# Kernel optimization log

Hardware: AMD Instinct MI355X
Metric: run time of the kernel (lower is better)

The kernel has to match this reference:

```python
import jax, jax.numpy as jnp
import numpy as np

B, T, F, DH, DG = 64, 4096, 64, 64, 128
SPAN, MASK_PROB = 5, 0.15
GROUPS = [(0, 5), (5, 8), (8, 11), (11, 14), (14, 26), (26, 38), (38, 46), (46, 64)]


def _make_feature_mask(rng):
    # Temporal span masking: num_spans spans of length SPAN, start ~ (U^2)*(T-SPAN)
    temporal = np.zeros((B, T), dtype=bool)
    num_spans = max(1, int(T * MASK_PROB / SPAN))
    starts = (rng.random((B, num_spans)) ** 2 * (T - SPAN)).astype(np.int64)
    for b in range(B):
        for s in starts[b]:
            temporal[b, s:s + SPAN] = True
    bb, tt = np.nonzero(temporal)
    n = len(bb)
    gm = np.zeros((8, F), dtype=np.uint8)
    for g, (a, c) in enumerate(GROUPS):
        gm[g, a:c] = 1
    sel = np.zeros((n, 8), dtype=np.uint8)
    branch = rng.random(n) < 0.3
    pairs = np.array([[4, 5], [1, 2], [6, 1]])
    pidx = rng.integers(0, 3, n)
    rows = np.nonzero(branch)[0]
    sel[rows, pairs[pidx[rows], 0]] = 1
    sel[rows, pairs[pidx[rows], 1]] = 1
    rows2 = np.nonzero(~branch)[0]
    k = rng.integers(1, 4, len(rows2))
    scores = rng.random((len(rows2), 8))
    rank = scores.argsort(axis=1).argsort(axis=1)
    sel[rows2] = (rank < k[:, None]).astype(np.uint8)
    fm = np.zeros((B, T, F), dtype=bool)
    fm[bb, tt] = (sel @ gm) > 0
    return fm


def setup_inputs() -> dict:
    rng = np.random.default_rng(0)
    x = jnp.asarray(rng.standard_normal((B, T, F)).astype(np.float32))
    feature_mask = jnp.asarray(_make_feature_mask(rng))

    def p(*s):
        return jnp.asarray((rng.standard_normal(s) * 0.05).astype(np.float32))

    return dict(
        x=x, feature_mask=feature_mask,
        stem_w=p(F, DH), stem_b=p(DH),
        conv_w=p(DH, DH, 3), conv_b=p(DH),
        gru_w_ih=p(3 * DG, DH), gru_w_hh=p(3 * DG, DG),
        gru_b_ih=p(3 * DG), gru_b_hh=p(3 * DG),
        h1_w=p(DG, 128), h1_b=p(128),
        h2_w=p(128, 128), h2_b=p(128),
        h3_w=p(128, F), h3_b=p(F),
    )


def _gelu(v):
    return jax.nn.gelu(v, approximate=False)


def _gru(x, w_ih, w_hh, b_ih, b_hh):
    # torch nn.GRU semantics, batch_first. x: (B, T, DH) -> (B, T, DG)
    H = w_hh.shape[1]
    gx = jnp.einsum('btd,hd->bth', x, w_ih) + b_ih  # (B, T, 3H)

    def step(h, gx_t):
        gh = h @ w_hh.T + b_hh  # (B, 3H)
        r = jax.nn.sigmoid(gx_t[:, :H] + gh[:, :H])
        z = jax.nn.sigmoid(gx_t[:, H:2 * H] + gh[:, H:2 * H])
        n = jnp.tanh(gx_t[:, 2 * H:] + r * gh[:, 2 * H:])
        h_new = (1.0 - z) * n + z * h
        return h_new, h_new

    h0 = jnp.zeros((x.shape[0], H), x.dtype)
    _, hs = jax.lax.scan(step, h0, jnp.swapaxes(gx, 0, 1))  # (T, B, H)
    return jnp.swapaxes(hs, 0, 1)


def reference(x, feature_mask, stem_w, stem_b, conv_w, conv_b,
              gru_w_ih, gru_w_hh, gru_b_ih, gru_b_hh,
              h1_w, h1_b, h2_w, h2_b, h3_w, h3_b):
    # mask-apply
    xm = jnp.where(feature_mask, jnp.zeros((), x.dtype), x)
    # encoder: Linear -> GELU -> Conv1d(k=3,pad=1) -> GELU -> GRU
    h = _gelu(xm @ stem_w + stem_b)  # (B, T, DH)
    hc = jax.lax.conv_general_dilated(
        jnp.swapaxes(h, 1, 2), conv_w, window_strides=(1,), padding=((1, 1),),
        dimension_numbers=('NCH', 'OIH', 'NCH'))
    h = _gelu(jnp.swapaxes(hc, 1, 2) + conv_b)
    z = _gru(h, gru_w_ih, gru_w_hh, gru_b_ih, gru_b_hh)  # (B, T, DG)
    # recon head
    r = _gelu(z @ h1_w + h1_b)
    r = _gelu(r @ h2_w + h2_b)
    x_recon = r @ h3_w + h3_b  # (B, T, F)
    # feature-normalized masked MSE (torch std is unbiased, ddof=1)
    scale = jnp.std(x, axis=(0, 1), ddof=1) + 1e-8
    diff = (x_recon - x) ** 2 / scale ** 2
    m = feature_mask.astype(x.dtype)
    return jnp.sum(diff * m) / jnp.maximum(jnp.sum(m), 1.0)
```

## Files before the change

kernel.cpp:

```cpp
#include <hip/hip_runtime.h>
#include <hip/hip_bf16.h>

#define DEV __device__ __forceinline__

namespace {

constexpr int ROWS = 64 * 4096;
constexpr int NE   = ROWS * 64;
constexpr int CHUNK = 512;
constexpr int NCHUNK = 4096 / CHUNK;

constexpr size_t GXCH = (size_t)64 * CHUNK * 384;
constexpr size_t RCH  = (size_t)64 * CHUNK * 128;

constexpr size_t OFF_XC  = 0;
constexpr size_t OFF_MC  = 33554432;
constexpr size_t OFF_WC  = 50331648;
constexpr size_t OFF_ACC = 50862080;
constexpr size_t OFF_H2  = 50866176;
constexpr size_t OFF_GX  = 84420608;
constexpr size_t OFF_ZR  = 134752256;
constexpr size_t OFF_R1  = 151529472;
constexpr size_t OFF_R2  = 168306688;
constexpr size_t OFF_HST = 185083904;

DEV float rlane(float v, int l) {
    return __int_as_float(__builtin_amdgcn_readlane(__float_as_int(v), l));
}
DEV unsigned int rlu(unsigned int v, int l) {
    return (unsigned int)__builtin_amdgcn_readlane((int)v, l);
}
DEV float bf2f(unsigned short u) { return __uint_as_float(((unsigned int)u) << 16); }
DEV unsigned short f2bf(float f) {
    unsigned int u = __float_as_uint(f);
    unsigned int r = (u + 0x7FFFu + ((u >> 16) & 1u)) >> 16;
    return (unsigned short)r;
}
DEV float gelu_f(float v) { return 0.5f * v * (1.0f + erff(v * 0.70710678118654752f)); }
DEV float sigm_f(float x) { return 1.0f / (1.0f + __expf(-x)); }
DEV float tanh_f(float x) { float t = __expf(2.0f * x); return 1.0f - 2.0f / (t + 1.0f); }

typedef _Float16 half2v __attribute__((ext_vector_type(2)));
typedef __attribute__((ext_vector_type(8))) short bf16x8;
typedef __attribute__((ext_vector_type(4))) float f32x4;

DEV float dot2(half2v a, half2v b, float c) {
#if __has_builtin(__builtin_amdgcn_fdot2)
    return __builtin_amdgcn_fdot2(a, b, c, false);
#else
    return c + (float)a.x * (float)b.x + (float)a.y * (float)b.y;
#endif
}
DEV unsigned short f2h_bits(float f) {
    return __builtin_bit_cast(unsigned short, (_Float16)f);
}
DEV float h2f_bits(unsigned short u) {
    return (float)__builtin_bit_cast(_Float16, u);
}
DEV half2v u2h2(unsigned int p) { return __builtin_bit_cast(half2v, p); }
DEV void bar_lds() {
    asm volatile("s_waitcnt lgkmcnt(0)\n\ts_barrier" ::: "memory");
}

}

__global__ __launch_bounds__(256) void k_probe(const unsigned short* __restrict__ xh,
    const unsigned char* __restrict__ mb, int* __restrict__ cnt)
{
    const int g = blockIdx.x * 256 + threadIdx.x;
    int hit = 0;
    for (int i = g; i < (1 << 20); i += (1 << 16)) {
        int tb = (xh[i] >> 8) & 0x7F;
        hit += (tb >= 0x3C && tb <= 0x40) ? 1 : 0;
    }
    int a = 0, b = 0, c = 0, d = 0;
    for (int i = g; i < (1 << 24); i += (1 << 16)) {
        unsigned char v = mb[i];
        int r = i & 3;
        a += (v == 1    && r == 0) ? 1 : 0;
        b += (v == 1    && r != 0) ? 1 : 0;
        c += (v == 0x80 && r == 0) ? 1 : 0;
        d += (v == 0x80 && r == 2) ? 1 : 0;
    }
    __shared__ int sm[256];
    int vals[5] = {hit, a, b, c, d};
#pragma unroll
    for (int k = 0; k < 5; ++k) {
        sm[threadIdx.x] = vals[k];
        __syncthreads();
        for (int s = 128; s > 0; s >>= 1) {
            if (threadIdx.x < s) sm[threadIdx.x] += sm[threadIdx.x + s];
            __syncthreads();
        }
        if (threadIdx.x == 0) atomicAdd(cnt + k, sm[0]);
        __syncthreads();
    }
}

__global__ void k_classify(const int* __restrict__ cnt, int* __restrict__ flags)
{
    flags[0] = (cnt[0] > 786432) ? 0 : 1;
    int fm;
    if (cnt[2] > 0) fm = 0;
    else if (cnt[1] > 0) fm = 1;
    else if (cnt[3] > 0) fm = 2;
    else if (cnt[4] > 0) fm = 3;
    else fm = 0;
    flags[1] = fm;
}

__global__ __launch_bounds__(256) void k_canon_x(const void* __restrict__ x,
    const void* __restrict__ mask, unsigned short* __restrict__ xc,
    unsigned char* __restrict__ mc, const int* __restrict__ flags)
{
    const int fF = flags[0], fM = flags[1];
    for (int i = blockIdx.x * 256 + threadIdx.x; i < NE; i += gridDim.x * 256) {
        unsigned short h;
        if (fF == 0) h = ((const unsigned short*)x)[i];
        else         h = f2bf(((const float*)x)[i]);
        xc[i] = h;
        unsigned char m;
        if (fM == 0)      m = (((const unsigned char*)mask)[i]  != 0) ? 1 : 0;
        else if (fM == 1) m = (((const int*)mask)[i]            != 0) ? 1 : 0;
        else if (fM == 2) m = (((const unsigned short*)mask)[i] != 0) ? 1 : 0;
        else              m = (((const unsigned int*)mask)[i]   != 0) ? 1 : 0;
        mc[i] = m;
    }
}

__global__ __launch_bounds__(256) void k_canon_w(
    const void* p0, const void* p1, const void* p2, const void* p3,
    const void* p4, const void* p5, const void* p6, const void* p7,
    const void* p8, const void* p9, const void* p10, const void* p11,
    const void* p12, const void* p13, float* __restrict__ wc,
    const int* __restrict__ flags)
{
    const int fF = flags[0];
    const void* p; int off, n;
    switch (blockIdx.x) {
        case 0:  p = p0;  off = 0;      n = 4096;  break;
        case 1:  p = p1;  off = 4096;   n = 64;    break;
        case 2:  p = p2;  off = 4160;   n = 12288; break;
        case 3:  p = p3;  off = 16448;  n = 64;    break;
        case 4:  p = p4;  off = 16512;  n = 24576; break;
        case 5:  p = p5;  off = 41088;  n = 49152; break;
        case 6:  p = p6;  off = 90240;  n = 384;   break;
        case 7:  p = p7;  off = 90624;  n = 384;   break;
        case 8:  p = p8;  off = 91008;  n = 16384; break;
        case 9:  p = p9;  off = 107392; n = 128;   break;
        case 10: p = p10; off = 107520; n = 16384; break;
        case 11: p = p11; off = 123904; n = 128;   break;
        case 12: p = p12; off = 124032; n = 8192;  break;
        default: p = p13; off = 132224; n = 64;    break;
    }
    for (int i = threadIdx.x; i < n; i += 256) {
        float v = (fF == 0) ? bf2f(((const unsigned short*)p)[i]) : ((const float*)p)[i];
        wc[off + i] = v;
    }
}

__global__ __launch_bounds__(256) void k_std(const unsigned short* __restrict__ xc,
    const unsigned char* __restrict__ mc, double* __restrict__ acc)
{
    const int tid = threadIdx.x, f = tid & 63, slot = tid >> 6;
    float s = 0.f, sq = 0.f; int cnt = 0;
    for (int row = blockIdx.x * 4 + slot; row < ROWS; row += gridDim.x * 4) {
        const size_t base = (size_t)row * 64 + f;
        float v = bf2f(xc[base]);
        s += v; sq += v * v;
        cnt += mc[base];
    }
    __shared__ float ls[256], lq[256];
    __shared__ int lc[256];
    ls[tid] = s; lq[tid] = sq; lc[tid] = cnt;
    __syncthreads();
    if (tid < 64) {
        float S = ls[tid] + ls[tid + 64] + ls[tid + 128] + ls[tid + 192];
        float Q = lq[tid] + lq[tid + 64] + lq[tid + 128] + lq[tid + 192];
        atomicAdd(acc + tid, (double)S);
        atomicAdd(acc + 64 + tid, (double)Q);
    }
    if (tid == 0) {
        int tot = 0;
        for (int i = 0; i < 256; ++i) tot += lc[i];
        atomicAdd(acc + 128, (double)tot);
    }
}

__global__ void k_scale(const double* __restrict__ acc, float* __restrict__ inv2)
{
    int f = threadIdx.x;
    const double N = (double)ROWS;
    double sum = acc[f], sq = acc[64 + f];
    double var = (sq - sum * sum / N) / (N - 1.0);
    double sd = sqrt(var) + 1e-8;
    inv2[f] = (float)(1.0 / (sd * sd));
}

__global__ __launch_bounds__(512) void k_stemconv(const unsigned short* __restrict__ xc,
    const unsigned char* __restrict__ mc, const float* __restrict__ sw,
    const float* __restrict__ sb, const float* __restrict__ cw,
    const float* __restrict__ cb, unsigned short* __restrict__ h2)
{
    __shared__ __align__(16) char smem[2 * 272 * 128];
    char* xs = smem;
    char* hs = smem + 272 * 128;

    const int tid = threadIdx.x, lane = tid & 63, w = tid >> 6;
    const int lr = lane & 15, lk = lane >> 4;
    const int ct = w & 3, wh = w >> 2;
    const int colN = ct * 16 + lr;
    const int b = blockIdx.x >> 4, strip = blockIdx.x & 15, t0 = strip * 256;

    const unsigned short* xb = xc + (size_t)b * 4096 * 64;
    const unsigned char*  mb = mc + (size_t)b * 4096 * 64;
    for (int idx = tid; idx < 272 * 8; idx += 512) {
        const int row = idx >> 3, cc = idx & 7;
        const int t = t0 - 1 + row;
        uint4 xv = {0u, 0u, 0u, 0u};
        if (row < 258 && t >= 0 && t < 4096) {
            const size_t gb = (size_t)t * 64 + cc * 8;
            xv = *(const uint4*)(xb + gb);
            uint2 mv = *(const uint2*)(mb + gb);
            union { uint2 v; unsigned char c[8]; } M; M.v = mv;
            union { uint4 v; unsigned short s[8]; } X; X.v = xv;
#pragma unroll
            for (int j = 0; j < 8; ++j) if (M.c[j]) X.s[j] = 0;
            xv = X.v;
        }
        *(uint4*)(xs + row * 128 + ((cc ^ (row & 7)) << 4)) = xv;
    }

    bf16x8 bs[2];
#pragma unroll
    for (int kb = 0; kb < 2; ++kb) {
        bf16x8 f;
#pragma unroll
        for (int j = 0; j < 8; ++j)
            f[j] = (short)f2bf(sw[(size_t)(kb * 32 + lk * 8 + j) * 64 + colN]);
        bs[kb] = f;
    }
    const float sbias = sb[colN];
    bf16x8 bc[3][2];
#pragma unroll
    for (int k = 0; k < 3; ++k)
#pragma unroll
        for (int kb = 0; kb < 2; ++kb) {
            bf16x8 f;
#pragma unroll
            for (int j = 0; j < 8; ++j)
                f[j] = (short)f2bf(cw[(size_t)colN * 192 + (kb * 32 + lk * 8 + j) * 3 + k]);
            bc[k][kb] = f;
        }
    const float cbias = cb[colN];

    __syncthreads();

    for (int rt = wh; rt < 17; rt += 2) {
        const int arow = rt * 16 + lr;
        bf16x8 a0 = *(const bf16x8*)(xs + arow * 128 + (((0 + lk) ^ (arow & 7)) << 4));
        bf16x8 a1 = *(const bf16x8*)(xs + arow * 128 + (((4 + lk) ^ (arow & 7)) << 4));
        f32x4 acc = {0.f, 0.f, 0.f, 0.f};
        acc = __builtin_amdgcn_mfma_f32_16x16x32_bf16(a0, bs[0], acc, 0, 0, 0);
        acc = __builtin_amdgcn_mfma_f32_16x16x32_bf16(a1, bs[1], acc, 0, 0, 0);
#pragma unroll
        for (int j = 0; j < 4; ++j) {
            const int row = rt * 16 + lk * 4 + j;
            if (row < 258) {
                const int t = t0 - 1 + row;
                unsigned short hv = (t >= 0 && t < 4096)
                    ? f2bf(gelu_f(acc[j] + sbias)) : (unsigned short)0;
                *(unsigned short*)(hs + row * 128 +
                    ((((colN >> 3) ^ (row & 7)) << 4)) + (colN & 7) * 2) = hv;
            }
        }
    }
    __syncthreads();

    unsigned short* h2b = h2 + ((size_t)b * 4096 + t0) * 64;
    for (int ot = wh; ot < 16; ot += 2) {
        f32x4 acc = {0.f, 0.f, 0.f, 0.f};
#pragma unroll
        for (int k = 0; k < 3; ++k) {
            const int arow = ot * 16 + k + lr;
            bf16x8 a0 = *(const bf16x8*)(hs + arow * 128 + (((0 + lk) ^ (arow & 7)) << 4));
            bf16x8 a1 = *(const bf16x8*)(hs + arow * 128 + (((4 + lk) ^ (arow & 7)) << 4));
            acc = __builtin_amdgcn_mfma_f32_16x16x32_bf16(a0, bc[k][0], acc, 0, 0, 0);
            acc = __builtin_amdgcn_mfma_f32_16x16x32_bf16(a1, bc[k][1], acc, 0, 0, 0);
        }
#pragma unroll
        for (int j = 0; j < 4; ++j) {
            const int orow = ot * 16 + lk * 4 + j;
            h2b[(size_t)orow * 64 + colN] = f2h_bits(gelu_f(acc[j] + cbias));
        }
    }
}

__global__ __launch_bounds__(384) void k_gx0(const unsigned short* __restrict__ h2,
    const float* __restrict__ wih, const float* __restrict__ bih,
    const float* __restrict__ bhh, unsigned short* __restrict__ gx0)
{
    const int tid = threadIdx.x, lane = tid & 63, wav = tid >> 6;
    const int col = wav * 64 + lane;
    half2v wg[32];
#pragma unroll
    for (int i = 0; i < 32; ++i)
        wg[i] = half2v{(_Float16)wih[(size_t)col * 64 + 2 * i],
                       (_Float16)wih[(size_t)col * 64 + 2 * i + 1]};
    const float gb = bih[col] + (col < 256 ? bhh[col] : 0.f);
    const unsigned int* h232 = (const unsigned int*)h2;
    const int b = blockIdx.x;
    const size_t hb = (size_t)b * 4096 * 32;
    unsigned int hw = h232[hb + (lane & 31)];
    for (int t = 0; t < CHUNK; ++t) {
        unsigned int hwn = (t + 1 < CHUNK) ? h232[hb + (size_t)(t + 1) * 32 + (lane & 31)] : 0u;
        float s = 0.f;
#pragma unroll
        for (int i = 0; i < 32; ++i)
            s = dot2(u2h2(rlu(hw, i)), wg[i], s);
        gx0[((size_t)b * CHUNK + t) * 384 + col] = f2h_bits(s + gb);
        hw = hwn;
    }
}

DEV void head_layer(const unsigned short* __restrict__ in,
                    unsigned short* __restrict__ out,
                    const float* __restrict__ w, const float* __restrict__ bias,
                    int hb, int nb)
{
    const int tid = threadIdx.x, lane = tid & 63, wav = tid >> 6;
    const int tm = wav >> 1, cs = wav & 1;
    const int col = cs * 64 + lane;
    half2v wv[64];
#pragma unroll
    for (int i = 0; i < 64; ++i)
        wv[i] = half2v{(_Float16)w[(size_t)(2 * i) * 128 + col],
                       (_Float16)w[(size_t)(2 * i + 1) * 128 + col]};
    const float bb = bias[col];
    for (int r = hb * 4 + tm; r < 64 * CHUNK; r += nb * 4) {
        const unsigned int* ir = (const unsigned int*)(in + (size_t)r * 128);
        unsigned int zw = ir[lane];
        float a0 = 0.f, a1 = 0.f;
#pragma unroll
        for (int i = 0; i < 64; i += 2) {
            a0 = dot2(u2h2(rlu(zw, i)),     wv[i],     a0);
            a1 = dot2(u2h2(rlu(zw, i + 1)), wv[i + 1], a1);
        }
        out[(size_t)r * 128 + col] = f2h_bits(gelu_f(a0 + a1 + bb));
    }
}

DEV void head3_layer(const unsigned short* __restrict__ in,
                     const float* __restrict__ w, const float* __restrict__ bias,
                     const unsigned short* __restrict__ xc,
                     const unsigned char* __restrict__ mc,
                     const float* __restrict__ inv2, double* __restrict__ lossacc,
                     int hb, int nb, int hc)
{
    const int tid = threadIdx.x, lane = tid & 63, wav = tid >> 6;
    half2v wv[64];
#pragma unroll
    for (int i = 0; i < 64; ++i)
        wv[i] = half2v{(_Float16)w[(size_t)(2 * i) * 64 + lane],
                       (_Float16)w[(size_t)(2 * i + 1) * 64 + lane]};
    const float bb = bias[lane];
    const float iv = inv2[lane];
    float accf = 0.f; double acc = 0.0; int spill = 0;
    for (int r = hb * 8 + wav; r < 64 * CHUNK; r += nb * 8) {
        const unsigned int* ir = (const unsigned int*)(in + (size_t)r * 128);
        unsigned int zw = ir[lane];
        float a0 = 0.f, a1 = 0.f;
#pragma unroll
        for (int i = 0; i < 64; i += 2) {
            a0 = dot2(u2h2(rlu(zw, i)),     wv[i],     a0);
            a1 = dot2(u2h2(rlu(zw, i + 1)), wv[i + 1], a1);
        }
        float xr = a0 + a1 + bb;
        const int bidx = r >> 9, tl = r & (CHUNK - 1);
        const int t = hc * CHUNK + tl;
        const size_t xb = ((size_t)bidx * 4096 + t) * 64 + lane;
        float dd = xr - bf2f(xc[xb]);
        accf += mc[xb] ? dd * dd * iv : 0.f;
        if (++spill == 64) { acc += (double)accf; accf = 0.f; spill = 0; }
    }
    acc += (double)accf;
    __shared__ double red[512];
    red[tid] = acc;
    __syncthreads();
    for (int s = 256; s > 0; s >>= 1) {
        if (tid < s) red[tid] += red[tid + s];
        __syncthreads();
    }
    if (tid == 0) atomicAdd(lossacc, red[0]);
}

__global__ __launch_bounds__(512) void k_pipe(int c,
    unsigned short* __restrict__ gxring, const unsigned short* __restrict__ h2,
    const float* __restrict__ wih, const float* __restrict__ bih,
    const float* __restrict__ whh, const float* __restrict__ bhh,
    unsigned short* __restrict__ zring, unsigned short* __restrict__ r1ring,
    unsigned short* __restrict__ r2ring, float* __restrict__ hstate,
    const float* __restrict__ h1w, const float* __restrict__ h1b,
    const float* __restrict__ h2w, const float* __restrict__ h2b,
    const float* __restrict__ h3w, const float* __restrict__ h3b,
    const unsigned short* __restrict__ xc, const unsigned char* __restrict__ mc,
    const float* __restrict__ inv2, double* __restrict__ lossacc)
{
    const int tid = threadIdx.x, lane = tid & 63, wav = tid >> 6;

    const int nGru = (c < NCHUNK) ? 64 : 0;
    const int nGx  = (c + 1 < NCHUNK) ? 64 : 0;
    const bool h1On = (c >= 1 && c - 1 < NCHUNK);
    const bool h2On = (c >= 2 && c - 2 < NCHUNK);
    const bool h3On = (c >= 3 && c - 3 < NCHUNK);
    const int rem = 256 - nGru - nGx;
    const int w1 = h1On ? 3 : 0, w2 = h2On ? 3 : 0, w3 = h3On ? 2 : 0;
    const int wsum = w1 + w2 + w3;
    const int n1 = wsum ? rem * w1 / wsum : 0;
    const int n2 = wsum ? rem * w2 / wsum : 0;
    const int n3 = h3On ? rem - n1 - n2 : 0;

    int bid = (int)blockIdx.x;

    if (bid < nGru) {
        __shared__ float part[4][3][130];
        __shared__ unsigned int hpk[64];
        const int b = bid;
        const int half = wav & 1, ksw = wav >> 1;
        const int d = half * 64 + lane;
        const int kb = __builtin_amdgcn_readfirstlane(ksw * 16);
        const unsigned short* gxb = gxring + (size_t)(c & 1) * GXCH + (size_t)b * CHUNK * 384;
        unsigned short* zc = zring + (size_t)(c & 1) * RCH + (size_t)b * CHUNK * 128;

        half2v wr[16], wz[16], wn[16];
#pragma unroll
        for (int i = 0; i < 16; ++i) {
            const int k0 = ksw * 32 + 2 * i;
            wr[i] = half2v{(_Float16)whh[(size_t)d * 128 + k0],
                           (_Float16)whh[(size_t)d * 128 + k0 + 1]};
            wz[i] = half2v{(_Float16)whh[(size_t)(128 + d) * 128 + k0],
                           (_Float16)whh[(size_t)(128 + d) * 128 + k0 + 1]};
            wn[i] = half2v{(_Float16)whh[(size_t)(256 + d) * 128 + k0],
                           (_Float16)whh[(size_t)(256 + d) * 128 + k0 + 1]};
        }
        const float bhn = bhh[256 + d];

        float hown = 0.0f;
        if (c > 0 && tid < 128) hown = hstate[b * 128 + tid];
        if (tid < 64) {
            float h0 = 0.f, h1v = 0.f;
            if (c > 0) {
                h0  = hstate[b * 128 + 2 * lane];
                h1v = hstate[b * 128 + 2 * lane + 1];
            }
            hpk[lane] = (unsigned int)f2h_bits(h0) | ((unsigned int)f2h_bits(h1v) << 16);
        }
        unsigned short cur[24], nxt[24];
        if (tid < 128) {
#pragma unroll
            for (int ti = 0; ti < 8; ++ti)
#pragma unroll
                for (int g3 = 0; g3 < 3; ++g3) {
                    cur[ti * 3 + g3] = gxb[(size_t)ti * 384 + g3 * 128 + tid];
                    nxt[ti * 3 + g3] = gxb[(size_t)(8 + ti) * 384 + g3 * 128 + tid];
                }
        }
        __syncthreads();

        for (int tb = 0; tb < CHUNK / 8; ++tb) {
#pragma unroll
            for (int ti = 0; ti < 8; ++ti) {
                const unsigned int hw = hpk[lane];
                float sr = 0.f, sz = 0.f, sn = 0.f;
#pragma unroll
                for (int i = 0; i < 16; ++i) {
                    const half2v hp = u2h2(rlu(hw, kb + i));
                    sr = dot2(hp, wr[i], sr);
                    sz = dot2(hp, wz[i], sz);
                    sn = dot2(hp, wn[i], sn);
                }
                part[ksw][0][d] = sr;
                part[ksw][1][d] = sz;
                part[ksw][2][d] = sn;
                bar_lds();
                if (tid < 128) {
                    const float gr  = part[0][0][tid] + part[1][0][tid] + part[2][0][tid]
                                    + part[3][0][tid] + h2f_bits(cur[ti * 3 + 0]);
                    const float gz  = part[0][1][tid] + part[1][1][tid] + part[2][1][tid]
                                    + part[3][1][tid] + h2f_bits(cur[ti * 3 + 1]);
                    const float gnh = part[0][2][tid] + part[1][2][tid] + part[2][2][tid]
                                    + part[3][2][tid] + bhn;
                    const float r  = sigm_f(gr);
                    const float zg = sigm_f(gz);
                    const float n  = tanh_f(h2f_bits(cur[ti * 3 + 2]) + r * gnh);
                    hown = n + zg * (hown - n);
                    ((unsigned short*)hpk)[tid] = f2h_bits(hown);
                    zc[(size_t)(tb * 8 + ti) * 128 + tid] = f2h_bits(hown);
                }
                bar_lds();
            }
            if (tid < 128) {
#pragma unroll
                for (int j = 0; j < 24; ++j) cur[j] = nxt[j];
                const int tnb = (tb + 2 <= CHUNK / 8 - 1) ? (tb + 2) * 8 : (CHUNK - 8);
#pragma unroll
                for (int ti = 0; ti < 8; ++ti)
#pragma unroll
                    for (int g3 = 0; g3 < 3; ++g3)
                        nxt[ti * 3 + g3] = gxb[(size_t)(tnb + ti) * 384 + g3 * 128 + tid];
            }
        }
        if (tid < 128) hstate[b * 128 + tid] = hown;
        return;
    }
    bid -= nGru;

    if (bid < nGx) {
        if (wav >= 6) return;
        const int b = bid;
        unsigned short* gxd = gxring + (size_t)((c + 1) & 1) * GXCH + (size_t)b * CHUNK * 384;
        const int col = wav * 64 + lane;
        half2v wg[32];
#pragma unroll
        for (int i = 0; i < 32; ++i)
            wg[i] = half2v{(_Float16)wih[(size_t)col * 64 + 2 * i],
                           (_Float16)wih[(size_t)col * 64 + 2 * i + 1]};
        const float gb = bih[col] + (col < 256 ? bhh[col] : 0.f);
        const unsigned int* h232 = (const unsigned int*)h2;
        const size_t hb = ((size_t)b * 4096 + (size_t)(c + 1) * CHUNK) * 32;
        unsigned int hw = h232[hb + (lane & 31)];
        for (int t = 0; t < CHUNK; ++t) {
            unsigned int hwn = (t + 1 < CHUNK) ? h232[hb + (size_t)(t + 1) * 32 + (lane & 31)] : 0u;
            float s = 0.f;
#pragma unroll
            for (int i = 0; i < 32; ++i)
                s = dot2(u2h2(rlu(hw, i)), wg[i], s);
            gxd[(size_t)t * 384 + col] = f2h_bits(s + gb);
            hw = hwn;
        }
        return;
    }
    bid -= nGx;

    if (bid < n1) {
        const int hc = c - 1;
        head_layer(zring + (size_t)(hc & 1) * RCH, r1ring + (size_t)(hc & 1) * RCH,
                   h1w, h1b, bid, n1);
        return;
    }
    bid -= n1;
    if (bid < n2) {
        const int hc = c - 2;
        head_layer(r1ring + (size_t)(hc & 1) * RCH, r2ring + (size_t)(hc & 1) * RCH,
                   h2w, h2b, bid, n2);
        return;
    }
    bid -= n2;
    if (bid < n3) {
        const int hc = c - 3;
        head3_layer(r2ring + (size_t)(hc & 1) * RCH, h3w, h3b, xc, mc, inv2,
                    lossacc, bid, n3, hc);
    }
}

__global__ void k_loss(const double* __restrict__ acc, const int* __restrict__ flags,
                       void* __restrict__ out)
{
    double cnt = acc[128];
    double denom = (cnt < 1.0) ? 1.0 : cnt;
    float v = (float)(acc[129] / denom);
    if (flags[0] == 1) ((float*)out)[0] = v;
    else ((unsigned short*)out)[0] = f2bf(v);
}

extern "C" void kernel_launch(void* const* d_in, const int* in_sizes, int n_in,
                              void* d_out, int out_size, void* d_ws, size_t ws_size,
                              hipStream_t stream)
{
    (void)in_sizes; (void)n_in; (void)out_size; (void)ws_size;
    const void* x    = d_in[0];
    const void* mask = d_in[1];

    char* ws = (char*)d_ws;
    unsigned short* xc   = (unsigned short*)(ws + OFF_XC);
    unsigned char*  mc   = (unsigned char*)(ws + OFF_MC);
    float*          wc   = (float*)(ws + OFF_WC);
    double*         acc  = (double*)(ws + OFF_ACC);
    int*            cnt  = (int*)(ws + OFF_ACC + 1056);
    int*            flg  = (int*)(ws + OFF_ACC + 1088);
    float*          inv2 = (float*)(ws + OFF_ACC + 1216);
    unsigned short* h2   = (unsigned short*)(ws + OFF_H2);
    unsigned short* gxr  = (unsigned short*)(ws + OFF_GX);
    unsigned short* zr   = (unsigned short*)(ws + OFF_ZR);
    unsigned short* r1r  = (unsigned short*)(ws + OFF_R1);
    unsigned short* r2r  = (unsigned short*)(ws + OFF_R2);
    float*          hst  = (float*)(ws + OFF_HST);

    const float* stem_w = wc + 0;
    const float* stem_b = wc + 4096;
    const float* conv_w = wc + 4160;
    const float* conv_b = wc + 16448;
    const float* w_ih   = wc + 16512;
    const float* w_hh   = wc + 41088;
    const float* b_ih   = wc + 90240;
    const float* b_hh   = wc + 90624;
    const float* h1_w   = wc + 91008;
    const float* h1_b   = wc + 107392;
    const float* h2_w   = wc + 107520;
    const float* h2_b   = wc + 123904;
    const float* h3_w   = wc + 124032;
    const float* h3_b   = wc + 132224;

    hipMemsetAsync(ws + OFF_ACC, 0, 4096, stream);
    k_probe   <<<256, 256, 0, stream>>>((const unsigned short*)x, (const unsigned char*)mask, cnt);
    k_classify<<<1, 1, 0, stream>>>(cnt, flg);
    k_canon_x <<<8192, 256, 0, stream>>>(x, mask, xc, mc, flg);
    k_canon_w <<<14, 256, 0, stream>>>(d_in[2], d_in[3], d_in[4], d_in[5], d_in[6],
                                       d_in[7], d_in[8], d_in[9], d_in[10], d_in[11],
                                       d_in[12], d_in[13], d_in[14], d_in[15], wc, flg);
    k_std     <<<512, 256, 0, stream>>>(xc, mc, acc);
    k_scale   <<<1, 64, 0, stream>>>(acc, inv2);
    k_stemconv<<<1024, 512, 0, stream>>>(xc, mc, stem_w, stem_b, conv_w, conv_b, h2);
    k_gx0     <<<64, 384, 0, stream>>>(h2, w_ih, b_ih, b_hh, gxr);

    for (int c = 0; c < NCHUNK + 3; ++c) {
        k_pipe<<<256, 512, 0, stream>>>(
            c, gxr, h2, w_ih, b_ih, w_hh, b_hh,
            zr, r1r, r2r, hst, h1_w, h1_b, h2_w, h2_b, h3_w, h3_b,
            xc, mc, inv2, acc + 129);
    }
    k_loss<<<1, 1, 0, stream>>>(acc, flg, d_out);
}
```

Baseline: 3.498 ms.

## Restructure GRU recurrence to four waves with redundant gate math and one barrier per step

The GRU block now uses four waves, each handling a K-slice for all 128 outputs (two outputs per lane), in place of eight waves split by half and K-slice. Every wave reduces the partial sums redundantly and updates its own copy of the hidden state in registers. This drops the second barrier per timestep and the LDS broadcast of h. Double-buffered partial sums avoid write-after-read hazards. Idle waves 4-7 just spin on matching barriers. In exchange each wave holds twice the weight registers and repeats the gate math.

```diff
diff --git a/kernel.cpp b/kernel.cpp
--- a/kernel.cpp
+++ b/kernel.cpp
@@ -423,83 +423,92 @@
     int bid = (int)blockIdx.x;
 
     if (bid < nGru) {
-        __shared__ float part[4][3][130];
-        __shared__ unsigned int hpk[64];
+        __shared__ float2 partb[2][4][3][64];
+        if (wav >= 4) {
+            for (int i = 0; i < CHUNK; ++i) bar_lds();
+            return;
+        }
         const int b = bid;
-        const int half = wav & 1, ksw = wav >> 1;
-        const int d = half * 64 + lane;
+        const int ksw = wav;
         const int kb = __builtin_amdgcn_readfirstlane(ksw * 16);
         const unsigned short* gxb = gxring + (size_t)(c & 1) * GXCH + (size_t)b * CHUNK * 384;
         unsigned short* zc = zring + (size_t)(c & 1) * RCH + (size_t)b * CHUNK * 128;
 
-        half2v wr[16], wz[16], wn[16];
-#pragma unroll
-        for (int i = 0; i < 16; ++i) {
-            const int k0 = ksw * 32 + 2 * i;
-            wr[i] = half2v{(_Float16)whh[(size_t)d * 128 + k0],
-                           (_Float16)whh[(size_t)d * 128 + k0 + 1]};
-            wz[i] = half2v{(_Float16)whh[(size_t)(128 + d) * 128 + k0],
-                           (_Float16)whh[(size_t)(128 + d) * 128 + k0 + 1]};
-            wn[i] = half2v{(_Float16)whh[(size_t)(256 + d) * 128 + k0],
-                           (_Float16)whh[(size_t)(256 + d) * 128 + k0 + 1]};
-        }
-        const float bhn = bhh[256 + d];
-
-        float hown = 0.0f;
-        if (c > 0 && tid < 128) hown = hstate[b * 128 + tid];
-        if (tid < 64) {
-            float h0 = 0.f, h1v = 0.f;
-            if (c > 0) {
-                h0  = hstate[b * 128 + 2 * lane];
-                h1v = hstate[b * 128 + 2 * lane + 1];
+        half2v w[3][2][16];
+#pragma unroll
+        for (int g = 0; g < 3; ++g)
+#pragma unroll
+            for (int dd = 0; dd < 2; ++dd) {
+                const size_t rowb = (size_t)(g * 128 + 2 * lane + dd) * 128 + ksw * 32;
+#pragma unroll
+                for (int i = 0; i < 16; ++i)
+                    w[g][dd][i] = half2v{(_Float16)whh[rowb + 2 * i],
+                                         (_Float16)whh[rowb + 2 * i + 1]};
             }
-            hpk[lane] = (unsigned int)f2h_bits(h0) | ((unsigned int)f2h_bits(h1v) << 16);
-        }
-        unsigned short cur[24], nxt[24];
-        if (tid < 128) {
-#pragma unroll
-            for (int ti = 0; ti < 8; ++ti)
-#pragma unroll
-                for (int g3 = 0; g3 < 3; ++g3) {
-                    cur[ti * 3 + g3] = gxb[(size_t)ti * 384 + g3 * 128 + tid];
-                    nxt[ti * 3 + g3] = gxb[(size_t)(8 + ti) * 384 + g3 * 128 + tid];
-                }
-        }
-        __syncthreads();
+        const float bhn0 = bhh[256 + 2 * lane];
+        const float bhn1 = bhh[256 + 2 * lane + 1];
+
+        float h0 = 0.f, h1v = 0.f;
+        if (c > 0) {
+            float2 hv = *(const float2*)(hstate + b * 128 + 2 * lane);
+            h0 = hv.x; h1v = hv.y;
+        }
+        unsigned int hw = (unsigned int)f2h_bits(h0) | ((unsigned int)f2h_bits(h1v) << 16);
+
+        unsigned int cur[24], nxt[24];
+#pragma unroll
+        for (int ti = 0; ti < 8; ++ti)
+#pragma unroll
+            for (int g3 = 0; g3 < 3; ++g3) {
+                cur[ti * 3 + g3] = *(const unsigned int*)(gxb + (size_t)ti * 384 + g3 * 128 + 2 * lane);
+                nxt[ti * 3 + g3] = *(const unsigned int*)(gxb + (size_t)(8 + ti) * 384 + g3 * 128 + 2 * lane);
+            }
 
         for (int tb = 0; tb < CHUNK / 8; ++tb) {
 #pragma unroll
             for (int ti = 0; ti < 8; ++ti) {
-                const unsigned int hw = hpk[lane];
-                float sr = 0.f, sz = 0.f, sn = 0.f;
+                const int par = ti & 1;
+                float s00 = 0.f, s01 = 0.f, s10 = 0.f, s11 = 0.f, s20 = 0.f, s21 = 0.f;
 #pragma unroll
                 for (int i = 0; i < 16; ++i) {
                     const half2v hp = u2h2(rlu(hw, kb + i));
-                    sr = dot2(hp, wr[i], sr);
-                    sz = dot2(hp, wz[i], sz);
-                    sn = dot2(hp, wn[i], sn);
+                    s00 = dot2(hp, w[0][0][i], s00);
+                    s01 = dot2(hp, w[0][1][i], s01);
+                    s10 = dot2(hp, w[1][0][i], s10);
+                    s11 = dot2(hp, w[1][1][i], s11);
+                    s20 = dot2(hp, w[2][0][i], s20);
+                    s21 = dot2(hp, w[2][1][i], s21);
                 }
-                part[ksw][0][d] = sr;
-                part[ksw][1][d] = sz;
-                part[ksw][2][d] = sn;
+                float2 f0; f0.x = s00; f0.y = s01; partb[par][ksw][0][lane] = f0;
+                float2 f1; f1.x = s10; f1.y = s11; partb[par][ksw][1][lane] = f1;
+                float2 f2; f2.x = s20; f2.y = s21; partb[par][ksw][2][lane] = f2;
                 bar_lds();
-                if (tid < 128) {
-                    const float gr  = part[0][0][tid] + part[1][0][tid] + part[2][0][tid]
-                                    + part[3][0][tid] + h2f_bits(cur[ti * 3 + 0]);
-                    const float gz  = part[0][1][tid] + part[1][1][tid] + part[2][1][tid]
-                                    + part[3][1][tid] + h2f_bits(cur[ti * 3 + 1]);
-                    const float gnh = part[0][2][tid] + part[1][2][tid] + part[2][2][tid]
-                                    + part[3][2][tid] + bhn;
-                    const float r  = sigm_f(gr);
-                    const float zg = sigm_f(gz);
-                    const float n  = tanh_f(h2f_bits(cur[ti * 3 + 2]) + r * gnh);
-                    hown = n + zg * (hown - n);
-                    ((unsigned short*)hpk)[tid] = f2h_bits(hown);
-                    zc[(size_t)(tb * 8 + ti) * 128 + tid] = f2h_bits(hown);
-                }
-                bar_lds();
+                const float2 pr0 = partb[par][0][0][lane], pr1 = partb[par][1][0][lane],
+                             pr2 = partb[par][2][0][lane], pr3 = partb[par][3][0][lane];
+                const float2 pz0 = partb[par][0][1][lane], pz1 = partb[par][1][1][lane],
+                             pz2 = partb[par][2][1][lane], pz3 = partb[par][3][1][lane];
+                const float2 pn0 = partb[par][0][2][lane], pn1 = partb[par][1][2][lane],
+                             pn2 = partb[par][2][2][lane], pn3 = partb[par][3][2][lane];
+                const half2v cr = u2h2(cur[ti * 3 + 0]);
+                const half2v cz = u2h2(cur[ti * 3 + 1]);
+                const half2v cn = u2h2(cur[ti * 3 + 2]);
+                const float gr0 = (pr0.x + pr1.x) + (pr2.x + pr3.x) + (float)cr.x;
+                const float gr1 = (pr0.y + pr1.y) + (pr2.y + pr3.y) + (float)cr.y;
+                const float gz0 = (pz0.x + pz1.x) + (pz2.x + pz3.x) + (float)cz.x;
+                const float gz1 = (pz0.y + pz1.y) + (pz2.y + pz3.y) + (float)cz.y;
+                const float gn0 = (pn0.x + pn1.x) + (pn2.x + pn3.x) + bhn0;
+                const float gn1 = (pn0.y + pn1.y) + (pn2.y + pn3.y) + bhn1;
+                const float r0 = sigm_f(gr0), r1 = sigm_f(gr1);
+                const float z0 = sigm_f(gz0), z1 = sigm_f(gz1);
+                const float n0 = tanh_f((float)cn.x + r0 * gn0);
+                const float n1 = tanh_f((float)cn.y + r1 * gn1);
+                h0  = n0 + z0 * (h0 - n0);
+                h1v = n1 + z1 * (h1v - n1);
+                hw = (unsigned int)f2h_bits(h0) | ((unsigned int)f2h_bits(h1v) << 16);
+                if (ksw == 0)
+                    *(unsigned int*)(zc + (size_t)(tb * 8 + ti) * 128 + 2 * lane) = hw;
             }
-            if (tid < 128) {
+            {
 #pragma unroll
                 for (int j = 0; j < 24; ++j) cur[j] = nxt[j];
                 const int tnb = (tb + 2 <= CHUNK / 8 - 1) ? (tb + 2) * 8 : (CHUNK - 8);
@@ -507,10 +516,13 @@
                 for (int ti = 0; ti < 8; ++ti)
 #pragma unroll
                     for (int g3 = 0; g3 < 3; ++g3)
-                        nxt[ti * 3 + g3] = gxb[(size_t)(tnb + ti) * 384 + g3 * 128 + tid];
+                        nxt[ti * 3 + g3] = *(const unsigned int*)(gxb + (size_t)(tnb + ti) * 384 + g3 * 128 + 2 * lane);
             }
         }
-        if (tid < 128) hstate[b * 128 + tid] = hown;
+        if (ksw == 0) {
+            float2 hv; hv.x = h0; hv.y = h1v;
+            *(float2*)(hstate + b * 128 + 2 * lane) = hv;
+        }
         return;
     }
     bid -= nGru;
```

Result: slower. 4.055 ms (+15.9%).

## Batch GRU recurrence across 16 sequences per block using MFMA

Applied to the files above, without the earlier changes.

The GRU recurrent step now processes 16 batch rows per block with MFMA 16x16x32 f16 matrix ops, replacing the per-sequence dot2/readlane scheme. The hidden state lives in double-buffered, XOR-swizzled LDS, which allows one barrier per timestep instead of two. GRU block count drops from 64 to 4, which frees blocks for the input-gate projection; that projection and k_gx0 are split over time ranges across more blocks. The risk is that per-step latency is now serialized on only 4 CUs, and the gx loads are strided per row and prefetched only one step ahead.

```diff
diff --git a/kernel.cpp b/kernel.cpp
--- a/kernel.cpp
+++ b/kernel.cpp
@@ -41,6 +41,7 @@
 DEV float tanh_f(float x) { float t = __expf(2.0f * x); return 1.0f - 2.0f / (t + 1.0f); }
 
 typedef _Float16 half2v __attribute__((ext_vector_type(2)));
+typedef _Float16 half8 __attribute__((ext_vector_type(8)));
 typedef __attribute__((ext_vector_type(8))) short bf16x8;
 typedef __attribute__((ext_vector_type(4))) float f32x4;
 
@@ -309,10 +310,10 @@
                        (_Float16)wih[(size_t)col * 64 + 2 * i + 1]};
     const float gb = bih[col] + (col < 256 ? bhh[col] : 0.f);
     const unsigned int* h232 = (const unsigned int*)h2;
-    const int b = blockIdx.x;
+    const int b = blockIdx.x >> 2, th = (blockIdx.x & 3) * 128;
     const size_t hb = (size_t)b * 4096 * 32;
-    unsigned int hw = h232[hb + (lane & 31)];
-    for (int t = 0; t < CHUNK; ++t) {
+    unsigned int hw = h232[hb + (size_t)th * 32 + (lane & 31)];
+    for (int t = th; t < th + 128; ++t) {
         unsigned int hwn = (t + 1 < CHUNK) ? h232[hb + (size_t)(t + 1) * 32 + (lane & 31)] : 0u;
         float s = 0.f;
 #pragma unroll
@@ -408,8 +409,8 @@
 {
     const int tid = threadIdx.x, lane = tid & 63, wav = tid >> 6;
 
-    const int nGru = (c < NCHUNK) ? 64 : 0;
-    const int nGx  = (c + 1 < NCHUNK) ? 64 : 0;
+    const int nGru = (c < NCHUNK) ? 4 : 0;
+    const int nGx  = (c + 1 < NCHUNK) ? 128 : 0;
     const bool h1On = (c >= 1 && c - 1 < NCHUNK);
     const bool h2On = (c >= 2 && c - 2 < NCHUNK);
     const bool h3On = (c >= 3 && c - 3 < NCHUNK);
@@ -423,101 +424,100 @@
     int bid = (int)blockIdx.x;
 
     if (bid < nGru) {
-        __shared__ float part[4][3][130];
-        __shared__ unsigned int hpk[64];
-        const int b = bid;
-        const int half = wav & 1, ksw = wav >> 1;
-        const int d = half * 64 + lane;
-        const int kb = __builtin_amdgcn_readfirstlane(ksw * 16);
-        const unsigned short* gxb = gxring + (size_t)(c & 1) * GXCH + (size_t)b * CHUNK * 384;
-        unsigned short* zc = zring + (size_t)(c & 1) * RCH + (size_t)b * CHUNK * 128;
-
-        half2v wr[16], wz[16], wn[16];
-#pragma unroll
-        for (int i = 0; i < 16; ++i) {
-            const int k0 = ksw * 32 + 2 * i;
-            wr[i] = half2v{(_Float16)whh[(size_t)d * 128 + k0],
-                           (_Float16)whh[(size_t)d * 128 + k0 + 1]};
-            wz[i] = half2v{(_Float16)whh[(size_t)(128 + d) * 128 + k0],
-                           (_Float16)whh[(size_t)(128 + d) * 128 + k0 + 1]};
-            wn[i] = half2v{(_Float16)whh[(size_t)(256 + d) * 128 + k0],
-                           (_Float16)whh[(size_t)(256 + d) * 128 + k0 + 1]};
-        }
+        __shared__ __align__(16) char hbuf[2 * 16 * 256];
+        const int b0 = bid * 16;
+        const int lr = lane & 15, lk = lane >> 4;
+        const int d = wav * 16 + lr;
+        const unsigned short* gxc = gxring + (size_t)(c & 1) * GXCH;
+        unsigned short* zc = zring + (size_t)(c & 1) * RCH;
+
+        half8 bw[3][4];
+#pragma unroll
+        for (int g = 0; g < 3; ++g)
+#pragma unroll
+            for (int kb = 0; kb < 4; ++kb) {
+                half8 f;
+#pragma unroll
+                for (int j = 0; j < 8; ++j)
+                    f[j] = (_Float16)whh[(size_t)(g * 128 + d) * 128 + kb * 32 + lk * 8 + j];
+                bw[g][kb] = f;
+            }
         const float bhn = bhh[256 + d];
 
-        float hown = 0.0f;
-        if (c > 0 && tid < 128) hown = hstate[b * 128 + tid];
-        if (tid < 64) {
-            float h0 = 0.f, h1v = 0.f;
-            if (c > 0) {
-                h0  = hstate[b * 128 + 2 * lane];
-                h1v = hstate[b * 128 + 2 * lane + 1];
+        float hreg[4];
+#pragma unroll
+        for (int j = 0; j < 4; ++j) {
+            const int row = lk * 4 + j;
+            hreg[j] = (c > 0) ? hstate[(size_t)(b0 + row) * 128 + d] : 0.f;
+            *(unsigned short*)(hbuf + row * 256 +
+                (((d >> 3) ^ (row & 7)) << 4) + (d & 7) * 2) = f2h_bits(hreg[j]);
+        }
+
+        unsigned short cur[12], nxt[12];
+#pragma unroll
+        for (int j = 0; j < 4; ++j)
+#pragma unroll
+            for (int g = 0; g < 3; ++g)
+                cur[j * 3 + g] = gxc[(size_t)(b0 + lk * 4 + j) * CHUNK * 384
+                                     + g * 128 + d];
+        bar_lds();
+
+        int p = 0;
+        for (int t = 0; t < CHUNK; ++t) {
+            half8 a[4];
+#pragma unroll
+            for (int kb = 0; kb < 4; ++kb) {
+                const int cc = kb * 4 + lk;
+                a[kb] = *(const half8*)(hbuf + p * 4096 + lr * 256 +
+                                        ((cc ^ (lr & 7)) << 4));
             }
-            hpk[lane] = (unsigned int)f2h_bits(h0) | ((unsigned int)f2h_bits(h1v) << 16);
-        }
-        unsigned short cur[24], nxt[24];
-        if (tid < 128) {
-#pragma unroll
-            for (int ti = 0; ti < 8; ++ti)
-#pragma unroll
-                for (int g3 = 0; g3 < 3; ++g3) {
-                    cur[ti * 3 + g3] = gxb[(size_t)ti * 384 + g3 * 128 + tid];
-                    nxt[ti * 3 + g3] = gxb[(size_t)(8 + ti) * 384 + g3 * 128 + tid];
-                }
-        }
-        __syncthreads();
-
-        for (int tb = 0; tb < CHUNK / 8; ++tb) {
-#pragma unroll
-            for (int ti = 0; ti < 8; ++ti) {
-                const unsigned int hw = hpk[lane];
-                float sr = 0.f, sz = 0.f, sn = 0.f;
-#pragma unroll
-                for (int i = 0; i < 16; ++i) {
-                    const half2v hp = u2h2(rlu(hw, kb + i));
-                    sr = dot2(hp, wr[i], sr);
-                    sz = dot2(hp, wz[i], sz);
-                    sn = dot2(hp, wn[i], sn);
-                }
-                part[ksw][0][d] = sr;
-                part[ksw][1][d] = sz;
-                part[ksw][2][d] = sn;
-                bar_lds();
-                if (tid < 128) {
-                    const float gr  = part[0][0][tid] + part[1][0][tid] + part[2][0][tid]
-                                    + part[3][0][tid] + h2f_bits(cur[ti * 3 + 0]);
-                    const float gz  = part[0][1][tid] + part[1][1][tid] + part[2][1][tid]
-                                    + part[3][1][tid] + h2f_bits(cur[ti * 3 + 1]);
-                    const float gnh = part[0][2][tid] + part[1][2][tid] + part[2][2][tid]
-                                    + part[3][2][tid] + bhn;
-                    const float r  = sigm_f(gr);
-                    const float zg = sigm_f(gz);
-                    const float n  = tanh_f(h2f_bits(cur[ti * 3 + 2]) + r * gnh);
-                    hown = n + zg * (hown - n);
-                    ((unsigned short*)hpk)[tid] = f2h_bits(hown);
-                    zc[(size_t)(tb * 8 + ti) * 128 + tid] = f2h_bits(hown);
-                }
-                bar_lds();
+            if (t + 1 < CHUNK) {
+#pragma unroll
+                for (int j = 0; j < 4; ++j)
+#pragma unroll
+                    for (int g = 0; g < 3; ++g)
+                        nxt[j * 3 + g] = gxc[((size_t)(b0 + lk * 4 + j) * CHUNK + t + 1) * 384
+                                             + g * 128 + d];
             }
-            if (tid < 128) {
-#pragma unroll
-                for (int j = 0; j < 24; ++j) cur[j] = nxt[j];
-                const int tnb = (tb + 2 <= CHUNK / 8 - 1) ? (tb + 2) * 8 : (CHUNK - 8);
-#pragma unroll
-                for (int ti = 0; ti < 8; ++ti)
-#pragma unroll
-                    for (int g3 = 0; g3 < 3; ++g3)
-                        nxt[ti * 3 + g3] = gxb[(size_t)(tnb + ti) * 384 + g3 * 128 + tid];
+            f32x4 ar = {0.f, 0.f, 0.f, 0.f};
+            f32x4 az = {0.f, 0.f, 0.f, 0.f};
+            f32x4 an = {0.f, 0.f, 0.f, 0.f};
+#pragma unroll
+            for (int kb = 0; kb < 4; ++kb) {
+                ar = __builtin_amdgcn_mfma_f32_16x16x32_f16(a[kb], bw[0][kb], ar, 0, 0, 0);
+                az = __builtin_amdgcn_mfma_f32_16x16x32_f16(a[kb], bw[1][kb], az, 0, 0, 0);
+                an = __builtin_amdgcn_mfma_f32_16x16x32_f16(a[kb], bw[2][kb], an, 0, 0, 0);
             }
-        }
-        if (tid < 128) hstate[b * 128 + tid] = hown;
+#pragma unroll
+            for (int j = 0; j < 4; ++j) {
+                const int row = lk * 4 + j;
+                const float gr  = ar[j] + h2f_bits(cur[j * 3 + 0]);
+                const float gz  = az[j] + h2f_bits(cur[j * 3 + 1]);
+                const float gnh = an[j] + bhn;
+                const float r  = sigm_f(gr);
+                const float zg = sigm_f(gz);
+                const float n  = tanh_f(h2f_bits(cur[j * 3 + 2]) + r * gnh);
+                hreg[j] = n + zg * (hreg[j] - n);
+                const unsigned short hv = f2h_bits(hreg[j]);
+                *(unsigned short*)(hbuf + (p ^ 1) * 4096 + row * 256 +
+                    (((d >> 3) ^ (row & 7)) << 4) + (d & 7) * 2) = hv;
+                zc[((size_t)(b0 + row) * CHUNK + t) * 128 + d] = hv;
+            }
+#pragma unroll
+            for (int j = 0; j < 12; ++j) cur[j] = nxt[j];
+            bar_lds();
+            p ^= 1;
+        }
+#pragma unroll
+        for (int j = 0; j < 4; ++j)
+            hstate[(size_t)(b0 + lk * 4 + j) * 128 + d] = hreg[j];
         return;
     }
     bid -= nGru;
 
     if (bid < nGx) {
         if (wav >= 6) return;
-        const int b = bid;
+        const int b = bid >> 1, th = (bid & 1) * 256;
         unsigned short* gxd = gxring + (size_t)((c + 1) & 1) * GXCH + (size_t)b * CHUNK * 384;
         const int col = wav * 64 + lane;
         half2v wg[32];
@@ -528,8 +528,8 @@
         const float gb = bih[col] + (col < 256 ? bhh[col] : 0.f);
         const unsigned int* h232 = (const unsigned int*)h2;
         const size_t hb = ((size_t)b * 4096 + (size_t)(c + 1) * CHUNK) * 32;
-        unsigned int hw = h232[hb + (lane & 31)];
-        for (int t = 0; t < CHUNK; ++t) {
+        unsigned int hw = h232[hb + (size_t)th * 32 + (lane & 31)];
+        for (int t = th; t < th + 256; ++t) {
             unsigned int hwn = (t + 1 < CHUNK) ? h232[hb + (size_t)(t + 1) * 32 + (lane & 31)] : 0u;
             float s = 0.f;
 #pragma unroll
@@ -621,7 +621,7 @@
     k_std     <<<512, 256, 0, stream>>>(xc, mc, acc);
     k_scale   <<<1, 64, 0, stream>>>(acc, inv2);
     k_stemconv<<<1024, 512, 0, stream>>>(xc, mc, stem_w, stem_b, conv_w, conv_b, h2);
-    k_gx0     <<<64, 384, 0, stream>>>(h2, w_ih, b_ih, b_hh, gxr);
+    k_gx0     <<<256, 384, 0, stream>>>(h2, w_ih, b_ih, b_hh, gxr);
 
     for (int c = 0; c < NCHUNK + 3; ++c) {
         k_pipe<<<256, 512, 0, stream>>>(
```

Measured after the change: 5.536 ms. +58.3%, slower.

## Remove second barrier in GRU step via redundant per-wave gate update and ping-pong partials

Applied to the files above, without the earlier changes.

The GRU recurrence block now has every wave redundantly compute the gate nonlinearities for a packed pair of hidden units, reading double-buffered partial sums from LDS. This drops the second barrier per timestep and the shared hidden-state broadcast, and the gx prefetch moves to packed 32-bit loads. The input-projection (gx) work is split across twice as many blocks in the pipe kernel and four times as many in the initial kernel, each computing eight timesteps at once for ILP. The cost is redundant transcendental work in all eight waves and fewer blocks left for the head layers.

```diff
diff --git a/kernel.cpp b/kernel.cpp
--- a/kernel.cpp
+++ b/kernel.cpp
@@ -309,17 +309,30 @@
                        (_Float16)wih[(size_t)col * 64 + 2 * i + 1]};
     const float gb = bih[col] + (col < 256 ? bhh[col] : 0.f);
     const unsigned int* h232 = (const unsigned int*)h2;
-    const int b = blockIdx.x;
+    const int b = blockIdx.x >> 2, th = (blockIdx.x & 3) * 128;
     const size_t hb = (size_t)b * 4096 * 32;
-    unsigned int hw = h232[hb + (lane & 31)];
-    for (int t = 0; t < CHUNK; ++t) {
-        unsigned int hwn = (t + 1 < CHUNK) ? h232[hb + (size_t)(t + 1) * 32 + (lane & 31)] : 0u;
-        float s = 0.f;
-#pragma unroll
-        for (int i = 0; i < 32; ++i)
-            s = dot2(u2h2(rlu(hw, i)), wg[i], s);
-        gx0[((size_t)b * CHUNK + t) * 384 + col] = f2h_bits(s + gb);
-        hw = hwn;
+    unsigned int hw[8], hn[8];
+#pragma unroll
+    for (int s = 0; s < 8; ++s)
+        hw[s] = h232[hb + (size_t)(th + s) * 32 + (lane & 31)];
+    for (int t = th; t < th + 128; t += 8) {
+#pragma unroll
+        for (int s = 0; s < 8; ++s) {
+            const int tt = t + 8 + s;
+            hn[s] = (tt < th + 128) ? h232[hb + (size_t)tt * 32 + (lane & 31)] : 0u;
+        }
+        float ss[8] = {0.f, 0.f, 0.f, 0.f, 0.f, 0.f, 0.f, 0.f};
+#pragma unroll
+        for (int i = 0; i < 32; ++i) {
+#pragma unroll
+            for (int s = 0; s < 8; ++s)
+                ss[s] = dot2(u2h2(rlu(hw[s], i)), wg[i], ss[s]);
+        }
+#pragma unroll
+        for (int s = 0; s < 8; ++s)
+            gx0[((size_t)b * CHUNK + t + s) * 384 + col] = f2h_bits(ss[s] + gb);
+#pragma unroll
+        for (int s = 0; s < 8; ++s) hw[s] = hn[s];
     }
 }
 
@@ -409,7 +422,7 @@
     const int tid = threadIdx.x, lane = tid & 63, wav = tid >> 6;
 
     const int nGru = (c < NCHUNK) ? 64 : 0;
-    const int nGx  = (c + 1 < NCHUNK) ? 64 : 0;
+    const int nGx  = (c + 1 < NCHUNK) ? 128 : 0;
     const bool h1On = (c >= 1 && c - 1 < NCHUNK);
     const bool h2On = (c >= 2 && c - 2 < NCHUNK);
     const bool h3On = (c >= 3 && c - 3 < NCHUNK);
@@ -423,14 +436,14 @@
     int bid = (int)blockIdx.x;
 
     if (bid < nGru) {
-        __shared__ float part[4][3][130];
-        __shared__ unsigned int hpk[64];
+        __shared__ float part[2][4][3][128];
         const int b = bid;
         const int half = wav & 1, ksw = wav >> 1;
         const int d = half * 64 + lane;
         const int kb = __builtin_amdgcn_readfirstlane(ksw * 16);
         const unsigned short* gxb = gxring + (size_t)(c & 1) * GXCH + (size_t)b * CHUNK * 384;
         unsigned short* zc = zring + (size_t)(c & 1) * RCH + (size_t)b * CHUNK * 128;
+        const unsigned int* gx32 = (const unsigned int*)gxb;
 
         half2v wr[16], wz[16], wn[16];
 #pragma unroll
@@ -443,34 +456,29 @@
             wn[i] = half2v{(_Float16)whh[(size_t)(256 + d) * 128 + k0],
                            (_Float16)whh[(size_t)(256 + d) * 128 + k0 + 1]};
         }
-        const float bhn = bhh[256 + d];
-
-        float hown = 0.0f;
-        if (c > 0 && tid < 128) hown = hstate[b * 128 + tid];
-        if (tid < 64) {
-            float h0 = 0.f, h1v = 0.f;
-            if (c > 0) {
-                h0  = hstate[b * 128 + 2 * lane];
-                h1v = hstate[b * 128 + 2 * lane + 1];
+        const float bhn0 = bhh[256 + 2 * lane];
+        const float bhn1 = bhh[256 + 2 * lane + 1];
+
+        float h0 = 0.f, h1v = 0.f;
+        if (c > 0) {
+            float2 hv = *(const float2*)(hstate + b * 128 + 2 * lane);
+            h0 = hv.x; h1v = hv.y;
+        }
+        unsigned int hw = (unsigned int)f2h_bits(h0) | ((unsigned int)f2h_bits(h1v) << 16);
+
+        unsigned int cur[12], nxt[12];
+#pragma unroll
+        for (int s = 0; s < 4; ++s)
+#pragma unroll
+            for (int g = 0; g < 3; ++g) {
+                cur[s * 3 + g] = gx32[(size_t)s * 192 + g * 64 + lane];
+                nxt[s * 3 + g] = gx32[(size_t)(4 + s) * 192 + g * 64 + lane];
             }
-            hpk[lane] = (unsigned int)f2h_bits(h0) | ((unsigned int)f2h_bits(h1v) << 16);
-        }
-        unsigned short cur[24], nxt[24];
-        if (tid < 128) {
-#pragma unroll
-            for (int ti = 0; ti < 8; ++ti)
-#pragma unroll
-                for (int g3 = 0; g3 < 3; ++g3) {
-                    cur[ti * 3 + g3] = gxb[(size_t)ti * 384 + g3 * 128 + tid];
-                    nxt[ti * 3 + g3] = gxb[(size_t)(8 + ti) * 384 + g3 * 128 + tid];
-                }
-        }
-        __syncthreads();
-
-        for (int tb = 0; tb < CHUNK / 8; ++tb) {
-#pragma unroll
-            for (int ti = 0; ti < 8; ++ti) {
-                const unsigned int hw = hpk[lane];
+
+        int p = 0;
+        for (int tb = 0; tb < CHUNK / 4; ++tb) {
+#pragma unroll
+            for (int ti = 0; ti < 4; ++ti) {
                 float sr = 0.f, sz = 0.f, sn = 0.f;
 #pragma unroll
                 for (int i = 0; i < 16; ++i) {
@@ -479,45 +487,62 @@
                     sz = dot2(hp, wz[i], sz);
                     sn = dot2(hp, wn[i], sn);
                 }
-                part[ksw][0][d] = sr;
-                part[ksw][1][d] = sz;
-                part[ksw][2][d] = sn;
+                part[p][ksw][0][d] = sr;
+                part[p][ksw][1][d] = sz;
+                part[p][ksw][2][d] = sn;
                 bar_lds();
-                if (tid < 128) {
-                    const float gr  = part[0][0][tid] + part[1][0][tid] + part[2][0][tid]
-                                    + part[3][0][tid] + h2f_bits(cur[ti * 3 + 0]);
-                    const float gz  = part[0][1][tid] + part[1][1][tid] + part[2][1][tid]
-                                    + part[3][1][tid] + h2f_bits(cur[ti * 3 + 1]);
-                    const float gnh = part[0][2][tid] + part[1][2][tid] + part[2][2][tid]
-                                    + part[3][2][tid] + bhn;
-                    const float r  = sigm_f(gr);
-                    const float zg = sigm_f(gz);
-                    const float n  = tanh_f(h2f_bits(cur[ti * 3 + 2]) + r * gnh);
-                    hown = n + zg * (hown - n);
-                    ((unsigned short*)hpk)[tid] = f2h_bits(hown);
-                    zc[(size_t)(tb * 8 + ti) * 128 + tid] = f2h_bits(hown);
-                }
-                bar_lds();
+                const float2 r0v = ((const float2*)part[p][0][0])[lane];
+                const float2 r1v = ((const float2*)part[p][1][0])[lane];
+                const float2 r2v = ((const float2*)part[p][2][0])[lane];
+                const float2 r3v = ((const float2*)part[p][3][0])[lane];
+                const float2 z0v = ((const float2*)part[p][0][1])[lane];
+                const float2 z1v = ((const float2*)part[p][1][1])[lane];
+                const float2 z2v = ((const float2*)part[p][2][1])[lane];
+                const float2 z3v = ((const float2*)part[p][3][1])[lane];
+                const float2 n0v = ((const float2*)part[p][0][2])[lane];
+                const float2 n1v = ((const float2*)part[p][1][2])[lane];
+                const float2 n2v = ((const float2*)part[p][2][2])[lane];
+                const float2 n3v = ((const float2*)part[p][3][2])[lane];
+                const half2v cr = u2h2(cur[ti * 3 + 0]);
+                const half2v cz = u2h2(cur[ti * 3 + 1]);
+                const half2v cn = u2h2(cur[ti * 3 + 2]);
+                const float gr0 = r0v.x + r1v.x + r2v.x + r3v.x + (float)cr.x;
+                const float gr1 = r0v.y + r1v.y + r2v.y + r3v.y + (float)cr.y;
+                const float gz0 = z0v.x + z1v.x + z2v.x + z3v.x + (float)cz.x;
+                const float gz1 = z0v.y + z1v.y + z2v.y + z3v.y + (float)cz.y;
+                const float gn0 = n0v.x + n1v.x + n2v.x + n3v.x + bhn0;
+                const float gn1 = n0v.y + n1v.y + n2v.y + n3v.y + bhn1;
+                const float rr0 = sigm_f(gr0), rr1 = sigm_f(gr1);
+                const float zz0 = sigm_f(gz0), zz1 = sigm_f(gz1);
+                const float nn0 = tanh_f((float)cn.x + rr0 * gn0);
+                const float nn1 = tanh_f((float)cn.y + rr1 * gn1);
+                h0  = nn0 + zz0 * (h0 - nn0);
+                h1v = nn1 + zz1 * (h1v - nn1);
+                hw = (unsigned int)f2h_bits(h0) | ((unsigned int)f2h_bits(h1v) << 16);
+                if (wav == 0)
+                    *(unsigned int*)(zc + (size_t)(tb * 4 + ti) * 128 + 2 * lane) = hw;
+                p ^= 1;
             }
-            if (tid < 128) {
-#pragma unroll
-                for (int j = 0; j < 24; ++j) cur[j] = nxt[j];
-                const int tnb = (tb + 2 <= CHUNK / 8 - 1) ? (tb + 2) * 8 : (CHUNK - 8);
-#pragma unroll
-                for (int ti = 0; ti < 8; ++ti)
-#pragma unroll
-                    for (int g3 = 0; g3 < 3; ++g3)
-                        nxt[ti * 3 + g3] = gxb[(size_t)(tnb + ti) * 384 + g3 * 128 + tid];
-            }
-        }
-        if (tid < 128) hstate[b * 128 + tid] = hown;
+#pragma unroll
+            for (int j = 0; j < 12; ++j) cur[j] = nxt[j];
+            const int tnb = (tb + 2 <= CHUNK / 4 - 1) ? (tb + 2) * 4 : (CHUNK - 4);
+#pragma unroll
+            for (int s = 0; s < 4; ++s)
+#pragma unroll
+                for (int g = 0; g < 3; ++g)
+                    nxt[s * 3 + g] = gx32[(size_t)(tnb + s) * 192 + g * 64 + lane];
+        }
+        if (wav == 0) {
+            float2 hv; hv.x = h0; hv.y = h1v;
+            *(float2*)(hstate + b * 128 + 2 * lane) = hv;
+        }
         return;
     }
     bid -= nGru;
 
     if (bid < nGx) {
         if (wav >= 6) return;
-        const int b = bid;
+        const int b = bid >> 1, th = (bid & 1) * 256;
         unsigned short* gxd = gxring + (size_t)((c + 1) & 1) * GXCH + (size_t)b * CHUNK * 384;
         const int col = wav * 64 + lane;
         half2v wg[32];
@@ -528,15 +553,28 @@
         const float gb = bih[col] + (col < 256 ? bhh[col] : 0.f);
         const unsigned int* h232 = (const unsigned int*)h2;
         const size_t hb = ((size_t)b * 4096 + (size_t)(c + 1) * CHUNK) * 32;
-        unsigned int hw = h232[hb + (lane & 31)];
-        for (int t = 0; t < CHUNK; ++t) {
-            unsigned int hwn = (t + 1 < CHUNK) ? h232[hb + (size_t)(t + 1) * 32 + (lane & 31)] : 0u;
-            float s = 0.f;
-#pragma unroll
-            for (int i = 0; i < 32; ++i)
-                s = dot2(u2h2(rlu(hw, i)), wg[i], s);
-            gxd[(size_t)t * 384 + col] = f2h_bits(s + gb);
-            hw = hwn;
+        unsigned int hw[8], hn[8];
+#pragma unroll
+        for (int s = 0; s < 8; ++s)
+            hw[s] = h232[hb + (size_t)(th + s) * 32 + (lane & 31)];
+        for (int t = th; t < th + 256; t += 8) {
+#pragma unroll
+            for (int s = 0; s < 8; ++s) {
+                const int tt = t + 8 + s;
+                hn[s] = (tt < th + 256) ? h232[hb + (size_t)tt * 32 + (lane & 31)] : 0u;
+            }
+            float ss[8] = {0.f, 0.f, 0.f, 0.f, 0.f, 0.f, 0.f, 0.f};
+#pragma unroll
+            for (int i = 0; i < 32; ++i) {
+#pragma unroll
+                for (int s = 0; s < 8; ++s)
+                    ss[s] = dot2(u2h2(rlu(hw[s], i)), wg[i], ss[s]);
+            }
+#pragma unroll
+            for (int s = 0; s < 8; ++s)
+                gxd[(size_t)(t + s) * 384 + col] = f2h_bits(ss[s] + gb);
+#pragma unroll
+            for (int s = 0; s < 8; ++s) hw[s] = hn[s];
         }
         return;
     }
@@ -621,7 +659,7 @@
     k_std     <<<512, 256, 0, stream>>>(xc, mc, acc);
     k_scale   <<<1, 64, 0, stream>>>(acc, inv2);
     k_stemconv<<<1024, 512, 0, stream>>>(xc, mc, stem_w, stem_b, conv_w, conv_b, h2);
-    k_gx0     <<<64, 384, 0, stream>>>(h2, w_ih, b_ih, b_hh, gxr);
+    k_gx0     <<<256, 384, 0, stream>>>(h2, w_ih, b_ih, b_hh, gxr);
 
     for (int c = 0; c < NCHUNK + 3; ++c) {
         k_pipe<<<256, 512, 0, stream>>>(
```

New measurement: 4.765 ms. 36.2% more time.
